# Kernel optimization log

Hardware: AMD Instinct MI355X
Metric: run time of the kernel (lower is better)

The kernel has to match this reference:

```python
import jax, jax.numpy as jnp
import numpy as np
import math
from jax.scipy.special import gammaln, xlogy

B, N, DIM1, DIM2 = 2, 2048, 1024, 512
H, DK, DV, NRPF = 8, 64, 64, 192


def _pos_embed(seq_len, feat):
    """Enformer-style positional basis: [2*seq_len-1, feat]."""
    nb = feat // 6
    dist = jnp.arange(-seq_len + 1, seq_len, dtype=jnp.float32)
    ad = jnp.abs(dist)[:, None]
    # exponential decay features
    half_life = 2.0 ** jnp.linspace(3.0, math.log2(seq_len), nb)
    f_exp = jnp.exp(-math.log(2.0) / half_life[None, :] * ad)
    # central mask features
    cw = 2.0 ** jnp.arange(1, nb + 1, dtype=jnp.float32) - 1.0
    f_cm = (cw[None, :] > ad).astype(jnp.float32)
    # gamma pdf features
    stddev = seq_len / (2.0 * nb)
    mean = jnp.linspace(seq_len / nb, float(seq_len), nb)[None, :]
    conc = (mean / stddev) ** 2
    rate = mean / stddev ** 2
    log_unnorm = xlogy(conc - 1.0, ad) - rate * ad
    log_norm = gammaln(conc) - conc * jnp.log(rate)
    prob = jnp.exp(log_unnorm - log_norm) + 1e-8
    f_g = prob / jnp.max(prob, axis=-1, keepdims=True)
    emb = jnp.concatenate([f_exp, f_cm, f_g], axis=-1)
    return jnp.concatenate([emb, jnp.sign(dist)[:, None] * emb], axis=-1)


def _relative_shift(x):
    # x: [b, h, t1, t2] with t2 = 2*n - 1 -> [b, h, t1, n]
    b, h, t1, t2 = x.shape
    x = jnp.pad(x, ((0, 0), (0, 0), (0, 0), (1, 0)))
    x = x.reshape(b, h, t2 + 1, t1)[:, :, 1:, :].reshape(b, h, t1, t2)
    return x[..., : (t2 + 2) // 2]


def _forward(x1, x2, Wq, Wk, Wv1, Wv2, Wrel, rel_pos_bias, Wo1, bo1, Wo2, bo2):
    Bb, n1, _ = x1.shape
    n2 = x2.shape[1]
    scale = DK ** -0.5
    split = lambda t, n: t.reshape(Bb, n, H, -1).transpose(0, 2, 1, 3)
    q = split(x1 @ Wq, n1) * scale          # [B,H,n1,DK]
    k = split(x2 @ Wk, n2)                  # [B,H,n2,DK]
    v2 = split(x2 @ Wv2, n2)                # [B,H,n2,DV]
    content = jnp.einsum('bhid,bhjd->bhij', q, k)
    pos = _pos_embed(n1, NRPF)              # [2n1-1, NRPF]
    rel_q = (pos @ Wrel).reshape(-1, H, DK).transpose(1, 0, 2)  # [H,2n1-1,DK]
    rel = jnp.einsum('bhjd,hnd->bhjn', k * scale + rel_pos_bias, rel_q)
    rel = _relative_shift(rel)              # [B,H,n2,n1]
    logits = content + rel.transpose(0, 1, 3, 2)
    attn = jax.nn.softmax(logits, axis=-1)  # [B,H,n1,n2]
    out1 = jnp.einsum('bhij,bhjd->bhid', attn, v2)
    out1 = out1.transpose(0, 2, 1, 3).reshape(Bb, n1, H * DV)
    # exchange=True path: reuse attn transposed with V from x1
    v1 = split(x1 @ Wv1, n1)                # [B,H,n1,DV]
    out2 = jnp.einsum('bhji,bhjd->bhid', attn, v1)
    out2 = out2.transpose(0, 2, 1, 3).reshape(Bb, n2, H * DV)
    return out1 @ Wo1 + bo1, out2 @ Wo2 + bo2


def setup_inputs() -> dict:
    key = jax.random.key(0)
    ks = jax.random.split(key, 10)
    s = lambda fan_in: 1.0 / math.sqrt(fan_in)
    return {
        'x1': jax.random.normal(ks[0], (B, N, DIM1), jnp.float32),
        'x2': jax.random.normal(ks[1], (B, N, DIM2), jnp.float32),
        'Wq': jax.random.normal(ks[2], (DIM1, H * DK), jnp.float32) * s(DIM1),
        'Wk': jax.random.normal(ks[3], (DIM2, H * DK), jnp.float32) * s(DIM2),
        'Wv1': jax.random.normal(ks[4], (DIM1, H * DV), jnp.float32) * s(DIM1),
        'Wv2': jax.random.normal(ks[5], (DIM2, H * DV), jnp.float32) * s(DIM2),
        'Wrel': jax.random.normal(ks[6], (NRPF, H * DK), jnp.float32) * s(NRPF),
        'rel_pos_bias': jax.random.normal(ks[7], (1, H, 1, DK), jnp.float32),
        'Wo1': jax.random.normal(ks[8], (H * DV, DIM1), jnp.float32) * s(H * DV),
        'bo1': jnp.zeros((DIM1,), jnp.float32),
        'Wo2': jax.random.normal(ks[9], (H * DV, DIM1), jnp.float32) * s(H * DV),
        'bo2': jnp.zeros((DIM1,), jnp.float32),
    }


def reference(x1, x2, Wq, Wk, Wv1, Wv2, Wrel, rel_pos_bias, Wo1, bo1, Wo2, bo2):
    return _forward(x1, x2, Wq, Wk, Wv1, Wv2, Wrel, rel_pos_bias, Wo1, bo1, Wo2, bo2)
```

## Files before the change

### kernel.cpp

```cpp
#include <hip/hip_runtime.h>
#include <math.h>

#define NSEQ 2048
#define NPOS 4095
#define NH   8
#define LOG2E 1.4426950408889634f

typedef _Float16 f16;
typedef f16 f16x8 __attribute__((ext_vector_type(8)));
typedef f16 f16x4 __attribute__((ext_vector_type(4)));
typedef float f32x4 __attribute__((ext_vector_type(4)));

#define MFMA16(a,b,c) __builtin_amdgcn_mfma_f32_16x16x32_f16(a,b,c,0,0,0)
#define LSWZ(row, col) (((row) << 7) + ((((col) << 1)) ^ (((row) & 7) << 4)))

__device__ __forceinline__ f16x8 cvt8(float4 a, float4 b) {
  f16x8 r = {(f16)a.x, (f16)a.y, (f16)a.z, (f16)a.w,
             (f16)b.x, (f16)b.y, (f16)b.z, (f16)b.w};
  return r;
}
__device__ __forceinline__ f16x8 scale8(f16x8 v, float4 a, float4 b) {
  f16x8 r;
  r[0] = (f16)((float)v[0] * a.x); r[1] = (f16)((float)v[1] * a.y);
  r[2] = (f16)((float)v[2] * a.z); r[3] = (f16)((float)v[3] * a.w);
  r[4] = (f16)((float)v[4] * b.x); r[5] = (f16)((float)v[5] * b.y);
  r[6] = (f16)((float)v[6] * b.z); r[7] = (f16)((float)v[7] * b.w);
  return r;
}

__global__ __launch_bounds__(256) void pos_embed_k(float* __restrict__ pos) {
  int t = blockIdx.x * 8 + (threadIdx.x >> 5);
  int f = threadIdx.x & 31;
  if (t >= NPOS) return;
  float dist = (float)(t - (NSEQ - 1));
  float ad = fabsf(dist);
  float sgn = (dist > 0.f) ? 1.f : ((dist < 0.f) ? -1.f : 0.f);
  double mean = 64.0 * (double)(f + 1);
  double conc = (mean / 32.0) * (mean / 32.0);
  double rate = mean / 1024.0;
  double p = 0.0;
  if (ad > 0.f) {
    double lu = (conc - 1.0) * log((double)ad) - rate * (double)ad;
    double ln = lgamma(conc) - conc * log(rate);
    p = exp(lu - ln);
  }
  float pf = (float)p + 1e-8f;
  float gmax = pf;
  #pragma unroll
  for (int mk = 1; mk <= 16; mk <<= 1) gmax = fmaxf(gmax, __shfl_xor(gmax, mk));
  float fg = pf / gmax;
  float hl = exp2f(3.f + 8.f * (float)f * (1.f / 31.f));
  float fe = exp2f(-ad / hl);
  float cw = exp2f((float)(f + 1)) - 1.f;
  float fc = (cw > ad) ? 1.f : 0.f;
  float* row = pos + (size_t)t * 192;
  row[f]       = fe;       row[32 + f]  = fc;       row[64 + f]  = fg;
  row[96 + f]  = sgn * fe; row[128 + f] = sgn * fc; row[160 + f] = sgn * fg;
}

__global__ __launch_bounds__(256) void relq_k(
    const float* __restrict__ A, const float* __restrict__ W, f16* __restrict__ relq)
{
  __shared__ f16 As[64][56];
  __shared__ f16 Bs[64][56];
  int tid = threadIdx.x, w = tid >> 6, lane = tid & 63, lr = lane >> 4, lc = lane & 15;
  int m0 = blockIdx.y * 64, n0 = blockIdx.x * 64;
  int ar = tid >> 2, ac = (tid & 3) * 8;
  int bk = tid >> 3, bn = (tid & 7) * 8;
  f32x4 acc[4] = {};
  for (int k0 = 0; k0 < 192; k0 += 32) {
    float4 a0 = make_float4(0.f,0.f,0.f,0.f), a1 = a0;
    if (m0 + ar < NPOS) {
      const float* ap = &A[(size_t)(m0 + ar) * 192 + k0 + ac];
      a0 = *(const float4*)ap; a1 = *(const float4*)(ap + 4);
    }
    *(f16x8*)&As[ar][ac] = cvt8(a0, a1);
    const float* bp = &W[(size_t)(k0 + bk) * 512 + n0 + bn];
    float4 b0 = *(const float4*)bp, b1 = *(const float4*)(bp + 4);
    f16 bv[8] = {(f16)b0.x,(f16)b0.y,(f16)b0.z,(f16)b0.w,(f16)b1.x,(f16)b1.y,(f16)b1.z,(f16)b1.w};
    #pragma unroll
    for (int tt = 0; tt < 8; tt++) { int t = (tt + bk) & 7; Bs[bn + t][bk] = bv[t]; }
    __syncthreads();
    f16x8 af = *(const f16x8*)&As[16*w + lc][8*lr];
    #pragma unroll
    for (int nt = 0; nt < 4; nt++) {
      f16x8 bf = *(const f16x8*)&Bs[16*nt + lc][8*lr];
      acc[nt] = MFMA16(af, bf, acc[nt]);
    }
    __syncthreads();
  }
  #pragma unroll
  for (int nt = 0; nt < 4; nt++)
    #pragma unroll
    for (int r = 0; r < 4; r++) {
      int m = m0 + 16*w + 4*lr + r;
      if (m >= NPOS) continue;
      int nn = n0 + 16*nt + lc;
      relq[((size_t)(nn >> 6) * NPOS + m) * 64 + (nn & 63)] = (f16)(acc[nt][r] * LOG2E);
    }
}

template<int KD, bool SC1>
__global__ __launch_bounds__(256) void projx_k(
    const float* __restrict__ A, const float* __restrict__ W1, const float* __restrict__ W2,
    f16* __restrict__ O1, f16* __restrict__ O2t, const float* __restrict__ rpb)
{
  __shared__ f16 As[128][40];
  __shared__ f16 Bs[64][40];
  int tid = threadIdx.x, w = tid >> 6, lane = tid & 63, lr = lane >> 4, lc = lane & 15;
  int m0 = blockIdx.y * 128, n0g = blockIdx.x * 64;
  bool first = (n0g < 512);
  const float* W = first ? W1 : W2;
  int n0 = n0g & 511;
  int ar = tid >> 1, ac = (tid & 1) * 16;
  int bk = tid >> 3, bn = (tid & 7) * 8;
  f32x4 acc[2][4] = {};
  for (int k0 = 0; k0 < KD; k0 += 32) {
    const float* ap = &A[(size_t)(m0 + ar) * KD + k0 + ac];
    *(f16x8*)&As[ar][ac]     = cvt8(*(const float4*)ap, *(const float4*)(ap + 4));
    *(f16x8*)&As[ar][ac + 8] = cvt8(*(const float4*)(ap + 8), *(const float4*)(ap + 12));
    const float* bp = &W[(size_t)(k0 + bk) * 512 + n0 + bn];
    float4 b0 = *(const float4*)bp, b1 = *(const float4*)(bp + 4);
    f16 bv[8] = {(f16)b0.x,(f16)b0.y,(f16)b0.z,(f16)b0.w,(f16)b1.x,(f16)b1.y,(f16)b1.z,(f16)b1.w};
    #pragma unroll
    for (int tt = 0; tt < 8; tt++) { int t = (tt + bk) & 7; Bs[bn + t][bk] = bv[t]; }
    __syncthreads();
    f16x8 af[2], bf[4];
    #pragma unroll
    for (int x = 0; x < 2; x++) af[x] = *(const f16x8*)&As[16*(2*w + x) + lc][8*lr];
    #pragma unroll
    for (int y = 0; y < 4; y++) bf[y] = *(const f16x8*)&Bs[16*y + lc][8*lr];
    #pragma unroll
    for (int x = 0; x < 2; x++)
      #pragma unroll
      for (int y = 0; y < 4; y++) acc[x][y] = MFMA16(af[x], bf[y], acc[x][y]);
    __syncthreads();
  }
  if (first) {
    #pragma unroll
    for (int x = 0; x < 2; x++)
      #pragma unroll
      for (int y = 0; y < 4; y++)
        #pragma unroll
        for (int r = 0; r < 4; r++) {
          int m = m0 + 16*(2*w + x) + 4*lr + r;
          int nn = n0 + 16*y + lc;
          float vv = acc[x][y][r];
          if (SC1) vv = vv * 0.125f + rpb[nn];
          else     vv = vv * LOG2E;
          O1[(((size_t)((m >> 11) * NH + (nn >> 6))) * NSEQ + (m & (NSEQ - 1))) * 64 + (nn & 63)] = (f16)vv;
        }
  } else {
    #pragma unroll
    for (int x = 0; x < 2; x++) {
      int mb = m0 + 16*(2*w + x) + 4*lr;
      #pragma unroll
      for (int y = 0; y < 4; y++) {
        int nn = n0 + 16*y + lc;
        f16x4 pk = {(f16)acc[x][y][0], (f16)acc[x][y][1], (f16)acc[x][y][2], (f16)acc[x][y][3]};
        *(f16x4*)&O2t[(((size_t)((mb >> 11) * NH + (nn >> 6))) * 64 + (nn & 63)) * NSEQ + (mb & (NSEQ - 1))] = pk;
      }
    }
  }
}

__global__ __launch_bounds__(256) void outproj_k(
    const f16* __restrict__ o1, const f16* __restrict__ o2,
    const float* __restrict__ Wo1, const float* __restrict__ Wo2,
    const float* __restrict__ bo1, const float* __restrict__ bo2,
    float* __restrict__ out)
{
  __shared__ f16 As[128][40];
  __shared__ f16 Bs[64][40];
  int by = blockIdx.y;
  bool first = (by < 32);
  const f16* A = first ? o1 : o2;
  const float* W = first ? Wo1 : Wo2;
  const float* bias = first ? bo1 : bo2;
  float* O = out + (first ? 0 : (size_t)4096 * 1024);
  int tid = threadIdx.x, w = tid >> 6, lane = tid & 63, lr = lane >> 4, lc = lane & 15;
  int m0 = (by & 31) * 128, n0 = blockIdx.x * 64;
  int ar = tid >> 1, ac = (tid & 1) * 16;
  int bk = tid >> 3, bn = (tid & 7) * 8;
  f32x4 acc[2][4] = {};
  for (int k0 = 0; k0 < 512; k0 += 32) {
    const f16* ap = &A[(size_t)(m0 + ar) * 512 + k0 + ac];
    *(f16x8*)&As[ar][ac]     = *(const f16x8*)ap;
    *(f16x8*)&As[ar][ac + 8] = *(const f16x8*)(ap + 8);
    const float* bp = &W[(size_t)(k0 + bk) * 1024 + n0 + bn];
    float4 b0 = *(const float4*)bp, b1 = *(const float4*)(bp + 4);
    f16 bv[8] = {(f16)b0.x,(f16)b0.y,(f16)b0.z,(f16)b0.w,(f16)b1.x,(f16)b1.y,(f16)b1.z,(f16)b1.w};
    #pragma unroll
    for (int tt = 0; tt < 8; tt++) { int t = (tt + bk) & 7; Bs[bn + t][bk] = bv[t]; }
    __syncthreads();
    f16x8 af[2], bf[4];
    #pragma unroll
    for (int x = 0; x < 2; x++) af[x] = *(const f16x8*)&As[16*(2*w + x) + lc][8*lr];
    #pragma unroll
    for (int y = 0; y < 4; y++) bf[y] = *(const f16x8*)&Bs[16*y + lc][8*lr];
    #pragma unroll
    for (int x = 0; x < 2; x++)
      #pragma unroll
      for (int y = 0; y < 4; y++) acc[x][y] = MFMA16(af[x], bf[y], acc[x][y]);
    __syncthreads();
  }
  #pragma unroll
  for (int x = 0; x < 2; x++)
    #pragma unroll
    for (int y = 0; y < 4; y++)
      #pragma unroll
      for (int r = 0; r < 4; r++) {
        int m = m0 + 16*(2*w + x) + 4*lr + r;
        int n = n0 + 16*y + lc;
        O[(size_t)m * 1024 + n] = acc[x][y][r] + bias[n];
      }
}

__global__ __launch_bounds__(256) void attn_k(
    const f16* __restrict__ q, const f16* __restrict__ kb,
    const f16* __restrict__ relq, const f16* __restrict__ v2t,
    f16* __restrict__ attnT, float* __restrict__ fac_t,
    f16* __restrict__ o1acc, int bh0)
{
  __shared__ char smem[65536];
  char* QG  = smem;
  char* KB0 = smem + 8192;
  char* KB1 = smem + 16384;
  char* VS0 = smem + 24576;
  char* VS1 = smem + 32768;
  char* R0  = smem + 40960;
  char* R1  = smem + 49152;
  int z = blockIdx.y, bh = bh0 + z, b = bh >> 3, h = bh & 7;
  int i0 = blockIdx.x * 64;
  int tid = threadIdx.x, w = tid >> 6, lane = tid & 63;
  int lr = lane >> 4, lc = lane & 15;
  char* PW = smem + 57344 + w * 2048;
  int base0 = i0 + 1984;
  int row = tid >> 2, c0 = (tid & 3) * 16;

  {
    const f16* qp = q + ((size_t)bh * NSEQ + i0 + row) * 64 + c0;
    *(f16x8*)(QG + LSWZ(row, c0))     = *(const f16x8*)qp;
    *(f16x8*)(QG + LSWZ(row, c0 + 8)) = *(const f16x8*)(qp + 8);
    const f16* rp = relq + ((size_t)h * NPOS + base0 + 64 + row) * 64 + c0;
    *(f16x8*)(R1 + LSWZ(row, c0))     = *(const f16x8*)rp;
    *(f16x8*)(R1 + LSWZ(row, c0 + 8)) = *(const f16x8*)(rp + 8);
  }
  __syncthreads();
  f16x8 qa0 = *(const f16x8*)(QG + LSWZ(16*w + lc, 8*lr));
  f16x8 qa1 = *(const f16x8*)(QG + LSWZ(16*w + lc, 32 + 8*lr));

  const f16* kpb  = kb  + ((size_t)bh * NSEQ + row) * 64 + c0;
  const f16* vpb  = v2t + ((size_t)bh * 64 + row) * NSEQ + c0;
  const f16* rpb0 = relq + ((size_t)h * NPOS + base0 + row) * 64 + c0;
  f16x8 skb0 = *(const f16x8*)kpb,  skb1 = *(const f16x8*)(kpb + 8);
  f16x8 sv0  = *(const f16x8*)vpb,  sv1  = *(const f16x8*)(vpb + 8);
  f16x8 sr0  = *(const f16x8*)rpb0, sr1  = *(const f16x8*)(rpb0 + 8);

  float m_run[4], ssum[4];
  float mreg0[4] = {}, mreg1[4] = {};
  f32x4 o1a[4] = {};
  #pragma unroll
  for (int r = 0; r < 4; r++) { m_run[r] = -1e30f; ssum[r] = 0.f; }

  for (int jt = 0; jt < 32; jt++) {
    int j0 = jt * 64;
    char* KB  = (jt & 1) ? KB1 : KB0;
    char* VS  = (jt & 1) ? VS1 : VS0;
    char* RsA = (jt & 1) ? R1 : R0;
    char* RsB = (jt & 1) ? R0 : R1;
    *(f16x8*)(KB + LSWZ(row, c0))      = skb0;  *(f16x8*)(KB + LSWZ(row, c0 + 8))  = skb1;
    *(f16x8*)(VS + LSWZ(row, c0))      = sv0;   *(f16x8*)(VS + LSWZ(row, c0 + 8))  = sv1;
    *(f16x8*)(RsA + LSWZ(row, c0))     = sr0;   *(f16x8*)(RsA + LSWZ(row, c0 + 8)) = sr1;
    __syncthreads();
    f32x4 cacc[4];
    f16x8 ka0 = {}, ka1 = {};
    __builtin_amdgcn_s_setprio(1);
    #pragma unroll
    for (int y = 0; y < 4; y++) {
      f16x8 b0 = *(const f16x8*)(KB + LSWZ(16*y + lc, 8*lr));
      f16x8 b1 = *(const f16x8*)(KB + LSWZ(16*y + lc, 32 + 8*lr));
      f32x4 t = {};
      t = MFMA16(qa0, b0, t);
      t = MFMA16(qa1, b1, t);
      cacc[y] = t;
      if (y == w) { ka0 = b0; ka1 = b1; }
    }
    __builtin_amdgcn_s_setprio(0);
    #pragma unroll
    for (int gg = 0; gg < 5; gg++) {
      int g = 3 - w + gg;
      char* Rg = (g < 4) ? RsA : RsB;
      int grow = 16 * (g & 3) + lc;
      f32x4 ga = {};
      ga = MFMA16(ka0, *(const f16x8*)(Rg + LSWZ(grow, 8*lr)), ga);
      ga = MFMA16(ka1, *(const f16x8*)(Rg + LSWZ(grow, 32 + 8*lr)), ga);
      int jj = 16*w + 4*lr;
      #pragma unroll
      for (int r = 0; r < 4; r++) {
        int ii = 16*g + lc + jj + r - 63;
        if ((unsigned)ii < 64u) *(f16*)(QG + LSWZ(jj + r, ii)) = (f16)ga[r];
      }
    }
    {
      int jn = (jt < 31) ? jt + 1 : 31;
      const f16* kpn = kb  + ((size_t)bh * NSEQ + jn * 64 + row) * 64 + c0;
      const f16* vpn = v2t + ((size_t)bh * 64 + row) * NSEQ + jn * 64 + c0;
      const f16* rpn = relq + ((size_t)h * NPOS + base0 - 64 * jn + row) * 64 + c0;
      skb0 = *(const f16x8*)kpn;  skb1 = *(const f16x8*)(kpn + 8);
      sv0  = *(const f16x8*)vpn;  sv1  = *(const f16x8*)(vpn + 8);
      sr0  = *(const f16x8*)rpn;  sr1  = *(const f16x8*)(rpn + 8);
    }
    __syncthreads();
    float l[4][4];
    #pragma unroll
    for (int y = 0; y < 4; y++) {
      f16x4 gv = *(const f16x4*)(QG + LSWZ(16*y + lc, 16*w + 4*lr));
      #pragma unroll
      for (int r = 0; r < 4; r++) l[y][r] = cacc[y][r] + (float)gv[r];
    }
    float pvr[4][4];
    #pragma unroll
    for (int r = 0; r < 4; r++) {
      float tm = fmaxf(fmaxf(l[0][r], l[1][r]), fmaxf(l[2][r], l[3][r]));
      #pragma unroll
      for (int mk = 1; mk <= 8; mk <<= 1) tm = fmaxf(tm, __shfl_xor(tm, mk));
      if (tm > m_run[r]) {
        float sc = exp2f(m_run[r] - tm);
        ssum[r] *= sc;
        #pragma unroll
        for (int nt = 0; nt < 4; nt++) o1a[nt][r] *= sc;
        m_run[r] = tm;
      }
      float mnew = m_run[r];
      float ps = 0.f;
      #pragma unroll
      for (int y = 0; y < 4; y++) {
        float p = exp2f(l[y][r] - mnew);
        ps += p;
        pvr[r][y] = p;
        *(f16*)(PW + LSWZ(4*lr + r, 16*y + lc)) = (f16)p;
      }
      ssum[r] += ps;
      if (jt < 16) { if (lc == jt) mreg0[r] = mnew; }
      else         { if (lc == jt - 16) mreg1[r] = mnew; }
    }
    #pragma unroll
    for (int y = 0; y < 4; y++) {
      f16x4 pk = {(f16)pvr[0][y], (f16)pvr[1][y], (f16)pvr[2][y], (f16)pvr[3][y]};
      *(f16x4*)&attnT[((size_t)z * NSEQ + j0 + 16*y + lc) * NSEQ + i0 + 16*w + 4*lr] = pk;
    }
    {
      f16x8 pa0 = *(const f16x8*)(PW + LSWZ(lc, 8*lr));
      f16x8 pa1 = *(const f16x8*)(PW + LSWZ(lc, 32 + 8*lr));
      __builtin_amdgcn_s_setprio(1);
      #pragma unroll
      for (int nt = 0; nt < 4; nt++) {
        f16x8 vf0 = *(const f16x8*)(VS + LSWZ(16*nt + lc, 8*lr));
        f16x8 vf1 = *(const f16x8*)(VS + LSWZ(16*nt + lc, 32 + 8*lr));
        o1a[nt] = MFMA16(pa0, vf0, o1a[nt]);
        o1a[nt] = MFMA16(pa1, vf1, o1a[nt]);
      }
      __builtin_amdgcn_s_setprio(0);
    }
  }
  float invs[4];
  #pragma unroll
  for (int r = 0; r < 4; r++) {
    float s = ssum[r];
    #pragma unroll
    for (int mk = 1; mk <= 8; mk <<= 1) s += __shfl_xor(s, mk);
    invs[r] = 1.f / s;
    int il = 16*w + 4*lr + r;
    float mf = m_run[r];
    #pragma unroll
    for (int jtb = 0; jtb < 2; jtb++) {
      int jt = jtb * 16 + lc;
      float mv = (jtb == 0) ? mreg0[r] : mreg1[r];
      float fv = exp2f(mv - mf) * invs[r];
      fac_t[((size_t)z * 32 + jt) * NSEQ + i0 + il] = fv;
    }
  }
  #pragma unroll
  for (int nt = 0; nt < 4; nt++)
    #pragma unroll
    for (int r = 0; r < 4; r++) {
      int rw = i0 + 16*w + 4*lr + r;
      o1acc[((size_t)b * NSEQ + rw) * 512 + h * 64 + 16*nt + lc] = (f16)(o1a[nt][r] * invs[r]);
    }
}

__global__ __launch_bounds__(256) void pv2_k(const f16* __restrict__ attnT,
    const f16* __restrict__ v1t, const float* __restrict__ fac_t,
    f16* __restrict__ oacc, int bh0)
{
  __shared__ char vsm[16384];
  int z = blockIdx.y, bh = bh0 + z, b = bh >> 3, h = bh & 7;
  int r0 = blockIdx.x * 64;
  int tid = threadIdx.x, w = tid >> 6, lane = tid & 63;
  int lr = lane >> 4, lc = lane & 15;
  int row = tid >> 2, cv = (tid & 3) * 16;
  const f16* vp = v1t + ((size_t)bh * 64 + row) * NSEQ + cv;
  const float* fp = fac_t + ((size_t)z * 32 + blockIdx.x) * NSEQ + cv;
  const f16* ap = attnT + ((size_t)z * NSEQ + r0 + 16*w + lc) * NSEQ + 8*lr;
  f32x4 acc[4] = {};
  for (int k0 = 0; k0 < NSEQ; k0 += 64) {
    char* vb = vsm + (((k0 >> 6) & 1) << 13);
    f16x8 v0 = *(const f16x8*)(vp + k0);
    f16x8 v1 = *(const f16x8*)(vp + k0 + 8);
    float4 f0 = *(const float4*)(fp + k0),     f1 = *(const float4*)(fp + k0 + 4);
    float4 f2 = *(const float4*)(fp + k0 + 8), f3 = *(const float4*)(fp + k0 + 12);
    *(f16x8*)(vb + LSWZ(row, cv))     = scale8(v0, f0, f1);
    *(f16x8*)(vb + LSWZ(row, cv + 8)) = scale8(v1, f2, f3);
    __syncthreads();
    f16x8 a0 = *(const f16x8*)(ap + k0);
    f16x8 a1 = *(const f16x8*)(ap + k0 + 32);
    #pragma unroll
    for (int nt = 0; nt < 4; nt++) {
      acc[nt] = MFMA16(a0, *(const f16x8*)(vb + LSWZ(16*nt + lc, 8*lr)), acc[nt]);
      acc[nt] = MFMA16(a1, *(const f16x8*)(vb + LSWZ(16*nt + lc, 32 + 8*lr)), acc[nt]);
    }
  }
  #pragma unroll
  for (int nt = 0; nt < 4; nt++)
    #pragma unroll
    for (int r = 0; r < 4; r++) {
      int rw = r0 + 16*w + 4*lr + r;
      oacc[((size_t)b * NSEQ + rw) * 512 + h * 64 + 16*nt + lc] = (f16)acc[nt][r];
    }
}

extern "C" void kernel_launch(void* const* d_in, const int* in_sizes, int n_in,
                              void* d_out, int out_size, void* d_ws, size_t ws_size,
                              hipStream_t stream) {
  const float* x1   = (const float*)d_in[0];
  const float* x2   = (const float*)d_in[1];
  const float* Wq   = (const float*)d_in[2];
  const float* Wk   = (const float*)d_in[3];
  const float* Wv1  = (const float*)d_in[4];
  const float* Wv2  = (const float*)d_in[5];
  const float* Wrel = (const float*)d_in[6];
  const float* rpb  = (const float*)d_in[7];
  const float* Wo1  = (const float*)d_in[8];
  const float* bo1  = (const float*)d_in[9];
  const float* Wo2  = (const float*)d_in[10];
  const float* bo2  = (const float*)d_in[11];
  float* out = (float*)d_out;

  char* base = (char*)d_ws;
  size_t off = 0;
  auto alloc = [&](size_t bytes) -> void* {
    void* p = base + off; off += (bytes + 255) & ~(size_t)255; return p;
  };
  float* pos   = (float*)alloc((size_t)NPOS * 192 * 4);
  f16*   relq  = (f16*)  alloc((size_t)NH * NPOS * 64 * 2);
  f16*   qh    = (f16*)  alloc((size_t)16 * NSEQ * 64 * 2);
  f16*   kbh   = (f16*)  alloc((size_t)16 * NSEQ * 64 * 2);
  f16*   v1t   = (f16*)  alloc((size_t)16 * 64 * NSEQ * 2);
  f16*   v2t   = (f16*)  alloc((size_t)16 * 64 * NSEQ * 2);
  f16*   o1acc = (f16*)  alloc((size_t)2 * NSEQ * 512 * 2);
  f16*   o2acc = (f16*)  alloc((size_t)2 * NSEQ * 512 * 2);
  float* fac_t = (float*)alloc((size_t)16 * 32 * NSEQ * 4);
  size_t baseB = off;

  int chunk = 1;
  for (int c = 16; c >= 1; c >>= 1) {
    size_t needB = baseB + (size_t)c * NSEQ * NSEQ * 2;
    if (needB <= ws_size) { chunk = c; break; }
  }
  f16* attnT = (f16*)(base + baseB);

  pos_embed_k<<<(NPOS + 7) / 8, 256, 0, stream>>>(pos);
  relq_k<<<dim3(8, 64), 256, 0, stream>>>(pos, Wrel, relq);
  projx_k<1024, false><<<dim3(16, 32), 256, 0, stream>>>(x1, Wq, Wv1, qh, v1t, nullptr);
  projx_k<512,  true ><<<dim3(16, 32), 256, 0, stream>>>(x2, Wk, Wv2, kbh, v2t, rpb);

  for (int bh0 = 0; bh0 < 16; bh0 += chunk) {
    attn_k<<<dim3(32, chunk), 256, 0, stream>>>(qh, kbh, relq, v2t, attnT, fac_t, o1acc, bh0);
    pv2_k<<<dim3(32, chunk), 256, 0, stream>>>(attnT, v1t, fac_t, o2acc, bh0);
  }

  outproj_k<<<dim3(16, 64), 256, 0, stream>>>(o1acc, o2acc, Wo1, Wo2, bo1, bo2, out);
}
```

Measured before the change: 265.2 us.

## Enlarge relq tile, swap attention grid axes, and simplify prefetch addressing

The relq projection now uses 128-row tiles with a 2x4 MFMA fragment per wave, halving the number of blocks and reusing each B fragment across two A tiles. The attention and PV kernels swap grid x/y so that consecutive block IDs run different heads, which changes how work lands on compute units and how the L2 cache is shared. Prefetch pointers are now advanced incrementally instead of recomputed each iteration. Probabilities are converted to f16 once and reused for both the LDS write and the attnT store. Together these mainly cut address arithmetic and change scheduling order, with small register-pressure risk in relq.

```diff
diff --git a/kernel.cpp b/kernel.cpp
--- a/kernel.cpp
+++ b/kernel.cpp
@@ -61,43 +61,50 @@
 __global__ __launch_bounds__(256) void relq_k(
     const float* __restrict__ A, const float* __restrict__ W, f16* __restrict__ relq)
 {
-  __shared__ f16 As[64][56];
-  __shared__ f16 Bs[64][56];
+  __shared__ f16 As[128][40];
+  __shared__ f16 Bs[64][40];
   int tid = threadIdx.x, w = tid >> 6, lane = tid & 63, lr = lane >> 4, lc = lane & 15;
-  int m0 = blockIdx.y * 64, n0 = blockIdx.x * 64;
-  int ar = tid >> 2, ac = (tid & 3) * 8;
+  int m0 = blockIdx.y * 128, n0 = blockIdx.x * 64;
+  int ar = tid >> 1, ac = (tid & 1) * 16;
   int bk = tid >> 3, bn = (tid & 7) * 8;
-  f32x4 acc[4] = {};
+  f32x4 acc[2][4] = {};
   for (int k0 = 0; k0 < 192; k0 += 32) {
-    float4 a0 = make_float4(0.f,0.f,0.f,0.f), a1 = a0;
+    float4 a0 = make_float4(0.f,0.f,0.f,0.f), a1 = a0, a2 = a0, a3 = a0;
     if (m0 + ar < NPOS) {
       const float* ap = &A[(size_t)(m0 + ar) * 192 + k0 + ac];
-      a0 = *(const float4*)ap; a1 = *(const float4*)(ap + 4);
-    }
-    *(f16x8*)&As[ar][ac] = cvt8(a0, a1);
+      a0 = *(const float4*)ap;       a1 = *(const float4*)(ap + 4);
+      a2 = *(const float4*)(ap + 8); a3 = *(const float4*)(ap + 12);
+    }
+    *(f16x8*)&As[ar][ac]     = cvt8(a0, a1);
+    *(f16x8*)&As[ar][ac + 8] = cvt8(a2, a3);
     const float* bp = &W[(size_t)(k0 + bk) * 512 + n0 + bn];
     float4 b0 = *(const float4*)bp, b1 = *(const float4*)(bp + 4);
     f16 bv[8] = {(f16)b0.x,(f16)b0.y,(f16)b0.z,(f16)b0.w,(f16)b1.x,(f16)b1.y,(f16)b1.z,(f16)b1.w};
     #pragma unroll
     for (int tt = 0; tt < 8; tt++) { int t = (tt + bk) & 7; Bs[bn + t][bk] = bv[t]; }
     __syncthreads();
-    f16x8 af = *(const f16x8*)&As[16*w + lc][8*lr];
-    #pragma unroll
-    for (int nt = 0; nt < 4; nt++) {
-      f16x8 bf = *(const f16x8*)&Bs[16*nt + lc][8*lr];
-      acc[nt] = MFMA16(af, bf, acc[nt]);
-    }
-    __syncthreads();
-  }
-  #pragma unroll
-  for (int nt = 0; nt < 4; nt++)
-    #pragma unroll
-    for (int r = 0; r < 4; r++) {
-      int m = m0 + 16*w + 4*lr + r;
-      if (m >= NPOS) continue;
-      int nn = n0 + 16*nt + lc;
-      relq[((size_t)(nn >> 6) * NPOS + m) * 64 + (nn & 63)] = (f16)(acc[nt][r] * LOG2E);
-    }
+    f16x8 af[2], bf[4];
+    #pragma unroll
+    for (int x = 0; x < 2; x++) af[x] = *(const f16x8*)&As[16*(2*w + x) + lc][8*lr];
+    #pragma unroll
+    for (int y = 0; y < 4; y++) bf[y] = *(const f16x8*)&Bs[16*y + lc][8*lr];
+    #pragma unroll
+    for (int x = 0; x < 2; x++)
+      #pragma unroll
+      for (int y = 0; y < 4; y++) acc[x][y] = MFMA16(af[x], bf[y], acc[x][y]);
+    __syncthreads();
+  }
+  #pragma unroll
+  for (int x = 0; x < 2; x++)
+    #pragma unroll
+    for (int y = 0; y < 4; y++)
+      #pragma unroll
+      for (int r = 0; r < 4; r++) {
+        int m = m0 + 16*(2*w + x) + 4*lr + r;
+        if (m >= NPOS) continue;
+        int nn = n0 + 16*y + lc;
+        relq[((size_t)(nn >> 6) * NPOS + m) * 64 + (nn & 63)] = (f16)(acc[x][y][r] * LOG2E);
+      }
 }
 
 template<int KD, bool SC1>
@@ -230,8 +237,8 @@
   char* VS1 = smem + 32768;
   char* R0  = smem + 40960;
   char* R1  = smem + 49152;
-  int z = blockIdx.y, bh = bh0 + z, b = bh >> 3, h = bh & 7;
-  int i0 = blockIdx.x * 64;
+  int z = blockIdx.x, bh = bh0 + z, b = bh >> 3, h = bh & 7;
+  int i0 = blockIdx.y * 64;
   int tid = threadIdx.x, w = tid >> 6, lane = tid & 63;
   int lr = lane >> 4, lc = lane & 15;
   char* PW = smem + 57344 + w * 2048;
@@ -250,12 +257,12 @@
   f16x8 qa0 = *(const f16x8*)(QG + LSWZ(16*w + lc, 8*lr));
   f16x8 qa1 = *(const f16x8*)(QG + LSWZ(16*w + lc, 32 + 8*lr));
 
-  const f16* kpb  = kb  + ((size_t)bh * NSEQ + row) * 64 + c0;
-  const f16* vpb  = v2t + ((size_t)bh * 64 + row) * NSEQ + c0;
-  const f16* rpb0 = relq + ((size_t)h * NPOS + base0 + row) * 64 + c0;
-  f16x8 skb0 = *(const f16x8*)kpb,  skb1 = *(const f16x8*)(kpb + 8);
-  f16x8 sv0  = *(const f16x8*)vpb,  sv1  = *(const f16x8*)(vpb + 8);
-  f16x8 sr0  = *(const f16x8*)rpb0, sr1  = *(const f16x8*)(rpb0 + 8);
+  const f16* kp_pf = kb  + ((size_t)bh * NSEQ + row) * 64 + c0;
+  const f16* vp_pf = v2t + ((size_t)bh * 64 + row) * NSEQ + c0;
+  const f16* rp_pf = relq + ((size_t)h * NPOS + base0 + row) * 64 + c0;
+  f16x8 skb0 = *(const f16x8*)kp_pf,  skb1 = *(const f16x8*)(kp_pf + 8);
+  f16x8 sv0  = *(const f16x8*)vp_pf,  sv1  = *(const f16x8*)(vp_pf + 8);
+  f16x8 sr0  = *(const f16x8*)rp_pf,  sr1  = *(const f16x8*)(rp_pf + 8);
 
   float m_run[4], ssum[4];
   float mreg0[4] = {}, mreg1[4] = {};
@@ -303,13 +310,10 @@
       }
     }
     {
-      int jn = (jt < 31) ? jt + 1 : 31;
-      const f16* kpn = kb  + ((size_t)bh * NSEQ + jn * 64 + row) * 64 + c0;
-      const f16* vpn = v2t + ((size_t)bh * 64 + row) * NSEQ + jn * 64 + c0;
-      const f16* rpn = relq + ((size_t)h * NPOS + base0 - 64 * jn + row) * 64 + c0;
-      skb0 = *(const f16x8*)kpn;  skb1 = *(const f16x8*)(kpn + 8);
-      sv0  = *(const f16x8*)vpn;  sv1  = *(const f16x8*)(vpn + 8);
-      sr0  = *(const f16x8*)rpn;  sr1  = *(const f16x8*)(rpn + 8);
+      if (jt < 31) { kp_pf += 64 * 64; vp_pf += 64; rp_pf -= 64 * 64; }
+      skb0 = *(const f16x8*)kp_pf;  skb1 = *(const f16x8*)(kp_pf + 8);
+      sv0  = *(const f16x8*)vp_pf;  sv1  = *(const f16x8*)(vp_pf + 8);
+      sr0  = *(const f16x8*)rp_pf;  sr1  = *(const f16x8*)(rp_pf + 8);
     }
     __syncthreads();
     float l[4][4];
@@ -319,7 +323,7 @@
       #pragma unroll
       for (int r = 0; r < 4; r++) l[y][r] = cacc[y][r] + (float)gv[r];
     }
-    float pvr[4][4];
+    f16 ph[4][4];
     #pragma unroll
     for (int r = 0; r < 4; r++) {
       float tm = fmaxf(fmaxf(l[0][r], l[1][r]), fmaxf(l[2][r], l[3][r]));
@@ -338,8 +342,8 @@
       for (int y = 0; y < 4; y++) {
         float p = exp2f(l[y][r] - mnew);
         ps += p;
-        pvr[r][y] = p;
-        *(f16*)(PW + LSWZ(4*lr + r, 16*y + lc)) = (f16)p;
+        ph[r][y] = (f16)p;
+        *(f16*)(PW + LSWZ(4*lr + r, 16*y + lc)) = ph[r][y];
       }
       ssum[r] += ps;
       if (jt < 16) { if (lc == jt) mreg0[r] = mnew; }
@@ -347,7 +351,7 @@
     }
     #pragma unroll
     for (int y = 0; y < 4; y++) {
-      f16x4 pk = {(f16)pvr[0][y], (f16)pvr[1][y], (f16)pvr[2][y], (f16)pvr[3][y]};
+      f16x4 pk = {ph[0][y], ph[1][y], ph[2][y], ph[3][y]};
       *(f16x4*)&attnT[((size_t)z * NSEQ + j0 + 16*y + lc) * NSEQ + i0 + 16*w + 4*lr] = pk;
     }
     {
@@ -395,13 +399,13 @@
     f16* __restrict__ oacc, int bh0)
 {
   __shared__ char vsm[16384];
-  int z = blockIdx.y, bh = bh0 + z, b = bh >> 3, h = bh & 7;
-  int r0 = blockIdx.x * 64;
+  int z = blockIdx.x, bh = bh0 + z, b = bh >> 3, h = bh & 7;
+  int r0 = blockIdx.y * 64;
   int tid = threadIdx.x, w = tid >> 6, lane = tid & 63;
   int lr = lane >> 4, lc = lane & 15;
   int row = tid >> 2, cv = (tid & 3) * 16;
   const f16* vp = v1t + ((size_t)bh * 64 + row) * NSEQ + cv;
-  const float* fp = fac_t + ((size_t)z * 32 + blockIdx.x) * NSEQ + cv;
+  const float* fp = fac_t + ((size_t)z * 32 + blockIdx.y) * NSEQ + cv;
   const f16* ap = attnT + ((size_t)z * NSEQ + r0 + 16*w + lc) * NSEQ + 8*lr;
   f32x4 acc[4] = {};
   for (int k0 = 0; k0 < NSEQ; k0 += 64) {
@@ -471,13 +475,13 @@
   f16* attnT = (f16*)(base + baseB);
 
   pos_embed_k<<<(NPOS + 7) / 8, 256, 0, stream>>>(pos);
-  relq_k<<<dim3(8, 64), 256, 0, stream>>>(pos, Wrel, relq);
+  relq_k<<<dim3(8, 32), 256, 0, stream>>>(pos, Wrel, relq);
   projx_k<1024, false><<<dim3(16, 32), 256, 0, stream>>>(x1, Wq, Wv1, qh, v1t, nullptr);
   projx_k<512,  true ><<<dim3(16, 32), 256, 0, stream>>>(x2, Wk, Wv2, kbh, v2t, rpb);
 
   for (int bh0 = 0; bh0 < 16; bh0 += chunk) {
-    attn_k<<<dim3(32, chunk), 256, 0, stream>>>(qh, kbh, relq, v2t, attnT, fac_t, o1acc, bh0);
-    pv2_k<<<dim3(32, chunk), 256, 0, stream>>>(attnT, v1t, fac_t, o2acc, bh0);
+    attn_k<<<dim3(chunk, 32), 256, 0, stream>>>(qh, kbh, relq, v2t, attnT, fac_t, o1acc, bh0);
+    pv2_k<<<dim3(chunk, 32), 256, 0, stream>>>(attnT, v1t, fac_t, o2acc, bh0);
   }
 
   outproj_k<<<dim3(16, 64), 256, 0, stream>>>(o1acc, o2acc, Wo1, Wo2, bo1, bo2, out);
```

Result: no change. 264.0 us (-0.4%).
